# Performance work log

Hardware: AMD Instinct MI355X
Metric: run time of the kernel (lower is better)

The kernel has to match this reference:

```python
import jax, jax.numpy as jnp
import numpy as np

PILLAR_WH = np.array([0.16, 0.16], np.float32)
MAX_POINTS = 100
MAX_PILLARS = 12000
MIN_XYZ = np.array([-51.2, -51.2, -5.0], np.float32)
MAX_XYZ = np.array([51.2, 51.2, 3.0], np.float32)
PAD_VALUE = 0.0
NGRID = np.ceil((MAX_XYZ[:2] - MIN_XYZ[:2]) / PILLAR_WH).astype(np.int32)  # [640, 640]
WH_N = (2.0 * PILLAR_WH / (MAX_XYZ[:2] - MIN_XYZ[:2])).astype(np.float32)  # pillar size in normalized coords
MIN_XY_N = (MIN_XYZ[:2] / MAX_XYZ[:2]).astype(np.float32)  # = [-1, -1]


def setup_inputs() -> dict:
    key = jax.random.key(0)
    B, P = 4, 50000
    k1, k2, k3 = jax.random.split(key, 3)
    # x,y restricted to [-8, 8] m so occupied pillars (<=100x100=10000) <= max_pillars,
    # making the torch module's random pillar subsampling a deterministic no-op.
    xy = jax.random.uniform(k1, (B, P, 2), minval=-8.0, maxval=8.0, dtype=jnp.float32)
    z = jax.random.uniform(k2, (B, P, 1), minval=-5.0, maxval=3.0, dtype=jnp.float32)
    r = jax.random.uniform(k3, (B, P, 1), dtype=jnp.float32)
    return {"point_clouds": jnp.concatenate([xy, z, r], axis=-1)}


def _per_sample(pc, pidx):
    # pc: (P, 4) normalized points; pidx: (P,) int32 pillar ids
    P = pc.shape[0]
    u, inv = jnp.unique(pidx, size=MAX_PILLARS, fill_value=-1, return_inverse=True)
    counts = jax.ops.segment_sum(jnp.ones((P,), jnp.int32), inv, num_segments=MAX_PILLARS)
    sums = jax.ops.segment_sum(pc[:, :3], inv, num_segments=MAX_PILLARS)
    mean = sums / jnp.maximum(counts, 1).astype(pc.dtype)[:, None]
    # stable sort points by pillar id; rank = position within pillar
    order = jnp.argsort(inv)
    seg = inv[order]
    pts = pc[order]
    start = jnp.cumsum(counts) - counts  # exclusive prefix of counts
    rank = jnp.arange(P, dtype=jnp.int32) - start[seg]
    in_cap = rank < MAX_POINTS
    flat = jnp.where(in_cap, seg * MAX_POINTS + rank, MAX_PILLARS * MAX_POINTS)  # OOB -> dropped
    buf = jnp.zeros((MAX_PILLARS * MAX_POINTS, 4), pc.dtype).at[flat].set(pts, mode='drop')
    occ = jnp.zeros((MAX_PILLARS * MAX_POINTS,), bool).at[flat].set(True, mode='drop')
    buf = buf.reshape(MAX_PILLARS, MAX_POINTS, 4)
    occ = occ.reshape(MAX_PILLARS, MAX_POINTS)
    ij = jnp.stack([u % NGRID[0], u // NGRID[0]], axis=-1).astype(pc.dtype)
    centers = jnp.asarray(MIN_XY_N) + ij * jnp.asarray(WH_N) + jnp.asarray(WH_N) * 0.5
    feat_c = jnp.abs(buf[..., :3] - mean[:, None, :])  # |xyz - pillar mean|
    feat_p = centers[:, None, :] - buf[..., :2]        # pillar center offset
    out = jnp.concatenate([buf, feat_c, feat_p], axis=-1)  # (max_pillars, max_points, 9)
    out = jnp.where(occ[..., None], out, jnp.asarray(PAD_VALUE, pc.dtype))
    return out, u


def reference(point_clouds):
    pc = point_clouds
    xyz_n = 2.0 * (pc[..., :3] - jnp.asarray(MIN_XYZ)) / jnp.asarray(MAX_XYZ - MIN_XYZ) - 1.0
    pc_n = jnp.concatenate([xyz_n, pc[..., 3:]], axis=-1)
    ij = jnp.minimum(
        jnp.floor((xyz_n[..., :2] - jnp.asarray(MIN_XY_N)) / jnp.asarray(WH_N)),
        jnp.asarray(NGRID, xyz_n.dtype) - 1.0,
    ).astype(jnp.int32)
    pidx = ij[..., 1] * int(NGRID[0]) + ij[..., 0]
    out, pillars = jax.vmap(_per_sample)(pc_n, pidx)
    return out, pillars
```

## Files before the change

### kernel.cpp

```cpp
#include <hip/hip_runtime.h>

#define NB 4
#define GRID_X 640
#define NCELL (GRID_X*GRID_X)
#define NWORD (NCELL/32)
#define MAXPIL 12000
#define MAXPTS 100
#define SCAN_BLK 256
#define NBLKA (NWORD/SCAN_BLK)

typedef unsigned short u16;
typedef unsigned int   u32;

__device__ __forceinline__ float bf16rt(float f) {
    u32 u = __builtin_bit_cast(u32, f);
    u32 r = ((u + 0x7FFFu + ((u >> 16) & 1u)) >> 16) << 16;
    return __builtin_bit_cast(float, r);
}

__device__ __forceinline__ float opaquef(float x) { asm volatile("" : "+v"(x)); return x; }

#define R102 0.009765625f
#define RWH  320.000030517578125f
__device__ __host__ constexpr float WH_N_C() { return (2.0f*0.16f)/(51.2f-(-51.2f)); }

__device__ __forceinline__ float norm_x(float v) {
    float p = 2.0f*(v + 51.2f) * R102;
    return opaquef(p) - 1.0f;
}
__device__ __forceinline__ float norm_z(float v) {
    float p = 2.0f*(v + 5.0f) * 0.125f;
    return opaquef(p) - 1.0f;
}

__device__ __forceinline__ int cell_of(float xn, float yn) {
    float fx = fminf(fmaxf(floorf((xn + 1.0f) * RWH), 0.0f), 639.0f);
    float fy = fminf(fmaxf(floorf((yn + 1.0f) * RWH), 0.0f), 639.0f);
    return (int)fy * GRID_X + (int)fx;
}

__global__ void k_init(int4* __restrict__ zero4, int nz4,
                       float* __restrict__ pillars_f, int* __restrict__ slotCell, int npil) {
    int i = blockIdx.x*blockDim.x + threadIdx.x;
    if (i < nz4) zero4[i] = make_int4(0,0,0,0);
    if (i < npil) { pillars_f[i] = -1.0f; slotCell[i] = -1; }
}

__global__ void k_mask(const float4* __restrict__ pc, int P, u32* __restrict__ occMask) {
    int i = blockIdx.x*blockDim.x + threadIdx.x;
    if (i >= NB*P) return;
    float4 pt = pc[i];
    int cell = cell_of(norm_x(pt.x), norm_x(pt.y));
    int b = i / P;
    atomicOr(&occMask[b*NWORD + (cell >> 5)], 1u << (cell & 31));
}

__global__ void k_scanA(const u32* __restrict__ occMask, int* __restrict__ scanBlk) {
    __shared__ int lds[SCAN_BLK];
    int blk = blockIdx.x % NBLKA;
    int b   = blockIdx.x / NBLKA;
    int w   = blk*SCAN_BLK + threadIdx.x;
    lds[threadIdx.x] = __popc(occMask[b*NWORD + w]);
    __syncthreads();
    for (int d = SCAN_BLK/2; d > 0; d >>= 1) {
        if (threadIdx.x < d) lds[threadIdx.x] += lds[threadIdx.x + d];
        __syncthreads();
    }
    if (threadIdx.x == 0) scanBlk[b*NBLKA + blk] = lds[0];
}

__global__ void k_scanB(int* __restrict__ scanBlk) {
    int b = blockIdx.x;
    if (threadIdx.x == 0) {
        int acc = 0;
        for (int i = 0; i < NBLKA; i++) {
            int v = scanBlk[b*NBLKA + i];
            scanBlk[b*NBLKA + i] = acc;
            acc += v;
        }
    }
}

__global__ void k_scanC(const u32* __restrict__ occMask, const int* __restrict__ scanBlk,
                        int* __restrict__ wordPrefix, float* __restrict__ pillars_f,
                        int* __restrict__ slotCell) {
    __shared__ int lds[SCAN_BLK];
    int blk = blockIdx.x % NBLKA;
    int b   = blockIdx.x / NBLKA;
    int tid = threadIdx.x;
    int w   = blk*SCAN_BLK + tid;
    u32 m = occMask[b*NWORD + w];
    int pop = __popc(m);
    lds[tid] = pop;
    __syncthreads();
    for (int d = 1; d < SCAN_BLK; d <<= 1) {
        int t = (tid >= d) ? lds[tid - d] : 0;
        __syncthreads();
        lds[tid] += t;
        __syncthreads();
    }
    int prefix = scanBlk[b*NBLKA + blk] + lds[tid] - pop;
    wordPrefix[b*NWORD + w] = prefix;
    int wbase = w << 5;
    int slot = prefix;
    while (m) {
        int bit = __ffs(m) - 1;
        m &= m - 1;
        if (slot < MAXPIL) {
            int cell = wbase + bit;
            slotCell[b*MAXPIL + slot] = cell;
            pillars_f[b*MAXPIL + slot] = bf16rt((float)cell);
        }
        slot++;
    }
}

__global__ void k_scatter(const float4* __restrict__ pc, int P,
                          const u32* __restrict__ occMask, const int* __restrict__ wordPrefix,
                          int* __restrict__ slotCnt, u16* __restrict__ idx16) {
    int i = blockIdx.x*blockDim.x + threadIdx.x;
    if (i >= NB*P) return;
    int b = i / P;
    int p = i - b*P;
    float4 pt = pc[i];
    int cell = cell_of(norm_x(pt.x), norm_x(pt.y));
    int w = cell >> 5, bit = cell & 31;
    u32 m = occMask[b*NWORD + w];
    int slot = wordPrefix[b*NWORD + w] + __popc(m & ((1u << bit) - 1u));
    if (slot >= MAXPIL) return;
    int g = b*MAXPIL + slot;
    int pos = atomicAdd(&slotCnt[g], 1);
    if (pos < MAXPTS) idx16[(size_t)g*MAXPTS + pos] = (u16)p;
}

__global__ __launch_bounds__(64) void k_write(const float4* __restrict__ pc, int P,
                        const int* __restrict__ slotCell, const int* __restrict__ slotCnt,
                        const u16* __restrict__ idx16, float* __restrict__ out) {
    __shared__ __align__(16) float tile[MAXPTS*9];
    __shared__ int sIdx[MAXPTS];
    __shared__ float sx[MAXPTS], sy[MAXPTS], sz[MAXPTS], sr[MAXPTS];
    int g = blockIdx.x;
    int b = g / MAXPIL;
    int lane = threadIdx.x;
    float4* out4 = (float4*)out + (size_t)g*225;
    int u = slotCell[g];
    if (u < 0) {
        float4 z = make_float4(0.f,0.f,0.f,0.f);
        for (int i = lane; i < 225; i += 64) out4[i] = z;
        return;
    }
    int ntot = slotCnt[g];
    int n = min(ntot, MAXPTS);

    float4* t4 = (float4*)tile;
    for (int i = lane; i < 225; i += 64) t4[i] = make_float4(0.f,0.f,0.f,0.f);

    float ax = 0.f, ay = 0.f, az = 0.f;
    for (int j = lane; j < n; j += 64) {
        int p = idx16[(size_t)g*MAXPTS + j];
        sIdx[j] = p;
        float4 pt = pc[b*P + p];
        float xn = norm_x(pt.x);
        float yn = norm_x(pt.y);
        float zn = norm_z(pt.z);
        sx[j] = xn; sy[j] = yn; sz[j] = zn; sr[j] = pt.w;
        ax += xn; ay += yn; az += zn;
    }
    for (int msk = 1; msk < 64; msk <<= 1) {
        ax += __shfl_xor(ax, msk);
        ay += __shfl_xor(ay, msk);
        az += __shfl_xor(az, msk);
    }
    float den = (float)max(ntot, 1);
    float mx = ax/den, my = ay/den, mz = az/den;
    const float wh = WH_N_C();
    float cx = -1.0f + (float)(u % GRID_X)*wh + wh*0.5f;
    float cy = -1.0f + (float)(u / GRID_X)*wh + wh*0.5f;
    __syncthreads();

    for (int j = lane; j < n; j += 64) {
        int p = sIdx[j];
        int rk = 0;
        for (int k = 0; k < n; k++) rk += (sIdx[k] < p) ? 1 : 0;
        float xn = sx[j], yn = sy[j], zn = sz[j];
        float* e = &tile[rk*9];
        e[0] = xn; e[1] = yn; e[2] = zn; e[3] = sr[j];
        e[4] = fabsf(xn - mx); e[5] = fabsf(yn - my); e[6] = fabsf(zn - mz);
        e[7] = cx - xn; e[8] = cy - yn;
    }
    __syncthreads();
    for (int i = lane; i < 225; i += 64) out4[i] = t4[i];
}

extern "C" void kernel_launch(void* const* d_in, const int* in_sizes, int n_in,
                              void* d_out, int out_size, void* d_ws, size_t ws_size,
                              hipStream_t stream) {
    const float4* pc = (const float4*)d_in[0];
    int P = in_sizes[0] / (NB*4);
    float* out = (float*)d_out;
    float* pillars_f = out + (size_t)NB*MAXPIL*MAXPTS*9;

    u32* occMask   = (u32*)d_ws;
    int* slotCnt   = (int*)(occMask + NB*NWORD);
    int* wordPrefix= slotCnt + NB*MAXPIL;
    int* scanBlk   = wordPrefix + NB*NWORD;
    int* slotCell  = scanBlk + 256;
    u16* idx16     = (u16*)(slotCell + NB*MAXPIL);

    int nzero = NB*NWORD + NB*MAXPIL;
    int nz4 = nzero / 4;
    int initThreads = nz4 > NB*MAXPIL ? nz4 : NB*MAXPIL;

    k_init<<<(initThreads+255)/256, 256, 0, stream>>>((int4*)occMask, nz4, pillars_f, slotCell, NB*MAXPIL);
    k_mask<<<(NB*P+255)/256, 256, 0, stream>>>(pc, P, occMask);
    k_scanA<<<NB*NBLKA, SCAN_BLK, 0, stream>>>(occMask, scanBlk);
    k_scanB<<<NB, 64, 0, stream>>>(scanBlk);
    k_scanC<<<NB*NBLKA, SCAN_BLK, 0, stream>>>(occMask, scanBlk, wordPrefix, pillars_f, slotCell);
    k_scatter<<<(NB*P+255)/256, 256, 0, stream>>>(pc, P, occMask, wordPrefix, slotCnt, idx16);
    k_write<<<NB*MAXPIL, 64, 0, stream>>>(pc, P, slotCell, slotCnt, idx16, out);
}
```

Measured before the change: 227.1 us.

## Merge scan into single-block kernel, zero output upfront, one thread per pillar

The three-kernel scan becomes one kernel per batch with 256 threads, each handling 50 words serially, which cuts two launches. The whole output is zeroed in one bulk pass at the start. The write kernel now uses one thread per pillar instead of a 64-lane block per pillar, computing ranks serially and writing 9-float rows straight to global memory with no LDS tile. The risks are long serial loops per thread (O(n^2) rank, scan over 50 words with only 4 blocks) and uncoalesced scattered row stores.

After: 293.9 us. 29.4% more time.

```diff
diff --git a/kernel.cpp b/kernel.cpp
--- a/kernel.cpp
+++ b/kernel.cpp
@@ -6,8 +6,7 @@
 #define NWORD (NCELL/32)
 #define MAXPIL 12000
 #define MAXPTS 100
-#define SCAN_BLK 256
-#define NBLKA (NWORD/SCAN_BLK)
+#define WPT (NWORD/256)
 
 typedef unsigned short u16;
 typedef unsigned int   u32;
@@ -39,11 +38,10 @@
     return (int)fy * GRID_X + (int)fx;
 }
 
-__global__ void k_init(int4* __restrict__ zero4, int nz4,
-                       float* __restrict__ pillars_f, int* __restrict__ slotCell, int npil) {
+__global__ void k_zero(float4* __restrict__ out4, int n4, int4* __restrict__ ws4, int nw4) {
     int i = blockIdx.x*blockDim.x + threadIdx.x;
-    if (i < nz4) zero4[i] = make_int4(0,0,0,0);
-    if (i < npil) { pillars_f[i] = -1.0f; slotCell[i] = -1; }
+    if (i < n4) out4[i] = make_float4(0.f,0.f,0.f,0.f);
+    if (i < nw4) ws4[i] = make_int4(0,0,0,0);
 }
 
 __global__ void k_mask(const float4* __restrict__ pc, int P, u32* __restrict__ occMask) {
@@ -55,63 +53,44 @@
     atomicOr(&occMask[b*NWORD + (cell >> 5)], 1u << (cell & 31));
 }
 
-__global__ void k_scanA(const u32* __restrict__ occMask, int* __restrict__ scanBlk) {
-    __shared__ int lds[SCAN_BLK];
-    int blk = blockIdx.x % NBLKA;
-    int b   = blockIdx.x / NBLKA;
-    int w   = blk*SCAN_BLK + threadIdx.x;
-    lds[threadIdx.x] = __popc(occMask[b*NWORD + w]);
+__global__ __launch_bounds__(256) void k_scan(const u32* __restrict__ occMask,
+                                              int* __restrict__ wordPrefix,
+                                              float* __restrict__ pillars_f,
+                                              int* __restrict__ slotCell) {
+    __shared__ int part[256];
+    int b = blockIdx.x, t = threadIdx.x;
+    for (int s = t; s < MAXPIL; s += 256) {
+        pillars_f[b*MAXPIL + s] = -1.0f;
+        slotCell[b*MAXPIL + s] = -1;
+    }
+    int base = b*NWORD + t*WPT;
+    int sum = 0;
+    #pragma unroll 10
+    for (int i = 0; i < WPT; i++) sum += __popc(occMask[base + i]);
+    part[t] = sum;
     __syncthreads();
-    for (int d = SCAN_BLK/2; d > 0; d >>= 1) {
-        if (threadIdx.x < d) lds[threadIdx.x] += lds[threadIdx.x + d];
+    for (int d = 1; d < 256; d <<= 1) {
+        int v = (t >= d) ? part[t - d] : 0;
+        __syncthreads();
+        part[t] += v;
         __syncthreads();
     }
-    if (threadIdx.x == 0) scanBlk[b*NBLKA + blk] = lds[0];
-}
-
-__global__ void k_scanB(int* __restrict__ scanBlk) {
-    int b = blockIdx.x;
-    if (threadIdx.x == 0) {
-        int acc = 0;
-        for (int i = 0; i < NBLKA; i++) {
-            int v = scanBlk[b*NBLKA + i];
-            scanBlk[b*NBLKA + i] = acc;
-            acc += v;
+    int prefix = part[t] - sum;
+    __syncthreads();
+    for (int i = 0; i < WPT; i++) {
+        u32 m = occMask[base + i];
+        wordPrefix[b*NWORD + t*WPT + i] = prefix;
+        int wbase = (t*WPT + i) << 5;
+        while (m) {
+            int bit = __ffs(m) - 1;
+            m &= m - 1;
+            if (prefix < MAXPIL) {
+                int cell = wbase + bit;
+                slotCell[b*MAXPIL + prefix] = cell;
+                pillars_f[b*MAXPIL + prefix] = bf16rt((float)cell);
+            }
+            prefix++;
         }
-    }
-}
-
-__global__ void k_scanC(const u32* __restrict__ occMask, const int* __restrict__ scanBlk,
-                        int* __restrict__ wordPrefix, float* __restrict__ pillars_f,
-                        int* __restrict__ slotCell) {
-    __shared__ int lds[SCAN_BLK];
-    int blk = blockIdx.x % NBLKA;
-    int b   = blockIdx.x / NBLKA;
-    int tid = threadIdx.x;
-    int w   = blk*SCAN_BLK + tid;
-    u32 m = occMask[b*NWORD + w];
-    int pop = __popc(m);
-    lds[tid] = pop;
-    __syncthreads();
-    for (int d = 1; d < SCAN_BLK; d <<= 1) {
-        int t = (tid >= d) ? lds[tid - d] : 0;
-        __syncthreads();
-        lds[tid] += t;
-        __syncthreads();
-    }
-    int prefix = scanBlk[b*NBLKA + blk] + lds[tid] - pop;
-    wordPrefix[b*NWORD + w] = prefix;
-    int wbase = w << 5;
-    int slot = prefix;
-    while (m) {
-        int bit = __ffs(m) - 1;
-        m &= m - 1;
-        if (slot < MAXPIL) {
-            int cell = wbase + bit;
-            slotCell[b*MAXPIL + slot] = cell;
-            pillars_f[b*MAXPIL + slot] = bf16rt((float)cell);
-        }
-        slot++;
     }
 }
 
@@ -133,63 +112,41 @@
     if (pos < MAXPTS) idx16[(size_t)g*MAXPTS + pos] = (u16)p;
 }
 
-__global__ __launch_bounds__(64) void k_write(const float4* __restrict__ pc, int P,
-                        const int* __restrict__ slotCell, const int* __restrict__ slotCnt,
-                        const u16* __restrict__ idx16, float* __restrict__ out) {
-    __shared__ __align__(16) float tile[MAXPTS*9];
-    __shared__ int sIdx[MAXPTS];
-    __shared__ float sx[MAXPTS], sy[MAXPTS], sz[MAXPTS], sr[MAXPTS];
-    int g = blockIdx.x;
+__global__ void k_rows(const float4* __restrict__ pc, int P,
+                       const int* __restrict__ slotCell, const int* __restrict__ slotCnt,
+                       const u16* __restrict__ idx16, float* __restrict__ out) {
+    int g = blockIdx.x*blockDim.x + threadIdx.x;
+    if (g >= NB*MAXPIL) return;
+    int u = slotCell[g];
+    if (u < 0) return;
     int b = g / MAXPIL;
-    int lane = threadIdx.x;
-    float4* out4 = (float4*)out + (size_t)g*225;
-    int u = slotCell[g];
-    if (u < 0) {
-        float4 z = make_float4(0.f,0.f,0.f,0.f);
-        for (int i = lane; i < 225; i += 64) out4[i] = z;
-        return;
-    }
     int ntot = slotCnt[g];
     int n = min(ntot, MAXPTS);
-
-    float4* t4 = (float4*)tile;
-    for (int i = lane; i < 225; i += 64) t4[i] = make_float4(0.f,0.f,0.f,0.f);
+    const u16* lst = idx16 + (size_t)g*MAXPTS;
 
     float ax = 0.f, ay = 0.f, az = 0.f;
-    for (int j = lane; j < n; j += 64) {
-        int p = idx16[(size_t)g*MAXPTS + j];
-        sIdx[j] = p;
-        float4 pt = pc[b*P + p];
-        float xn = norm_x(pt.x);
-        float yn = norm_x(pt.y);
-        float zn = norm_z(pt.z);
-        sx[j] = xn; sy[j] = yn; sz[j] = zn; sr[j] = pt.w;
-        ax += xn; ay += yn; az += zn;
-    }
-    for (int msk = 1; msk < 64; msk <<= 1) {
-        ax += __shfl_xor(ax, msk);
-        ay += __shfl_xor(ay, msk);
-        az += __shfl_xor(az, msk);
+    for (int j = 0; j < n; j++) {
+        float4 pt = pc[b*P + lst[j]];
+        ax += norm_x(pt.x); ay += norm_x(pt.y); az += norm_z(pt.z);
     }
     float den = (float)max(ntot, 1);
     float mx = ax/den, my = ay/den, mz = az/den;
     const float wh = WH_N_C();
     float cx = -1.0f + (float)(u % GRID_X)*wh + wh*0.5f;
     float cy = -1.0f + (float)(u / GRID_X)*wh + wh*0.5f;
-    __syncthreads();
 
-    for (int j = lane; j < n; j += 64) {
-        int p = sIdx[j];
+    float* pil = out + (size_t)g*900;
+    for (int j = 0; j < n; j++) {
+        int p = lst[j];
         int rk = 0;
-        for (int k = 0; k < n; k++) rk += (sIdx[k] < p) ? 1 : 0;
-        float xn = sx[j], yn = sy[j], zn = sz[j];
-        float* e = &tile[rk*9];
-        e[0] = xn; e[1] = yn; e[2] = zn; e[3] = sr[j];
+        for (int k = 0; k < n; k++) rk += (lst[k] < (u16)p) ? 1 : 0;
+        float4 pt = pc[b*P + p];
+        float xn = norm_x(pt.x), yn = norm_x(pt.y), zn = norm_z(pt.z);
+        float* e = pil + rk*9;
+        e[0] = xn; e[1] = yn; e[2] = zn; e[3] = pt.w;
         e[4] = fabsf(xn - mx); e[5] = fabsf(yn - my); e[6] = fabsf(zn - mz);
         e[7] = cx - xn; e[8] = cy - yn;
     }
-    __syncthreads();
-    for (int i = lane; i < 225; i += 64) out4[i] = t4[i];
 }
 
 extern "C" void kernel_launch(void* const* d_in, const int* in_sizes, int n_in,
@@ -203,19 +160,15 @@
     u32* occMask   = (u32*)d_ws;
     int* slotCnt   = (int*)(occMask + NB*NWORD);
     int* wordPrefix= slotCnt + NB*MAXPIL;
-    int* scanBlk   = wordPrefix + NB*NWORD;
-    int* slotCell  = scanBlk + 256;
+    int* slotCell  = wordPrefix + NB*NWORD;
     u16* idx16     = (u16*)(slotCell + NB*MAXPIL);
 
-    int nzero = NB*NWORD + NB*MAXPIL;
-    int nz4 = nzero / 4;
-    int initThreads = nz4 > NB*MAXPIL ? nz4 : NB*MAXPIL;
+    const int nOut4 = NB*MAXPIL*MAXPTS*9/4;
+    const int nWs4  = (NB*NWORD + NB*MAXPIL)/4;
 
-    k_init<<<(initThreads+255)/256, 256, 0, stream>>>((int4*)occMask, nz4, pillars_f, slotCell, NB*MAXPIL);
+    k_zero<<<(nOut4+255)/256, 256, 0, stream>>>((float4*)out, nOut4, (int4*)occMask, nWs4);
     k_mask<<<(NB*P+255)/256, 256, 0, stream>>>(pc, P, occMask);
-    k_scanA<<<NB*NBLKA, SCAN_BLK, 0, stream>>>(occMask, scanBlk);
-    k_scanB<<<NB, 64, 0, stream>>>(scanBlk);
-    k_scanC<<<NB*NBLKA, SCAN_BLK, 0, stream>>>(occMask, scanBlk, wordPrefix, pillars_f, slotCell);
+    k_scan<<<NB, 256, 0, stream>>>(occMask, wordPrefix, pillars_f, slotCell);
     k_scatter<<<(NB*P+255)/256, 256, 0, stream>>>(pc, P, occMask, wordPrefix, slotCnt, idx16);
-    k_write<<<NB*MAXPIL, 64, 0, stream>>>(pc, P, slotCell, slotCnt, idx16, out);
+    k_rows<<<(NB*MAXPIL+255)/256, 256, 0, stream>>>(pc, P, slotCell, slotCnt, idx16, out);
 }
```

## Fold block-offset scan into scanC, cache pillar ids, trim write-kernel LDS zeroing

Applied to the files above, without the earlier changes.

Drops the single-threaded k_scanB launch by having each k_scanC block sum the preceding block totals with a wavefront shuffle reduction. k_mask now stores each point's cell index, so k_scatter reads it instead of recomputing from the point cloud. k_write no longer stages normalized coordinates in LDS or zeroes the whole tile. It re-reads points from global memory, zero-fills only the unused tail, and pads with zeros on the store. This removes a serial launch and some LDS traffic, at the cost of an extra point-id buffer and repeated global gathers of points.

Measured after the change: 243.5 us. +7.2%, slower.

```diff
diff --git a/kernel.cpp b/kernel.cpp
--- a/kernel.cpp
+++ b/kernel.cpp
@@ -6,8 +6,7 @@
 #define NWORD (NCELL/32)
 #define MAXPIL 12000
 #define MAXPTS 100
-#define SCAN_BLK 256
-#define NBLKA (NWORD/SCAN_BLK)
+#define NBLKA (NWORD/256)
 
 typedef unsigned short u16;
 typedef unsigned int   u32;
@@ -39,91 +38,86 @@
     return (int)fy * GRID_X + (int)fx;
 }
 
-__global__ void k_init(int4* __restrict__ zero4, int nz4,
+__global__ void k_init(int4* __restrict__ ws4, int nw4,
                        float* __restrict__ pillars_f, int* __restrict__ slotCell, int npil) {
     int i = blockIdx.x*blockDim.x + threadIdx.x;
-    if (i < nz4) zero4[i] = make_int4(0,0,0,0);
+    if (i < nw4) ws4[i] = make_int4(0,0,0,0);
     if (i < npil) { pillars_f[i] = -1.0f; slotCell[i] = -1; }
 }
 
-__global__ void k_mask(const float4* __restrict__ pc, int P, u32* __restrict__ occMask) {
+__global__ void k_mask(const float4* __restrict__ pc, int P,
+                       u32* __restrict__ occMask, u32* __restrict__ pidxBuf) {
     int i = blockIdx.x*blockDim.x + threadIdx.x;
     if (i >= NB*P) return;
     float4 pt = pc[i];
     int cell = cell_of(norm_x(pt.x), norm_x(pt.y));
     int b = i / P;
     atomicOr(&occMask[b*NWORD + (cell >> 5)], 1u << (cell & 31));
-}
-
-__global__ void k_scanA(const u32* __restrict__ occMask, int* __restrict__ scanBlk) {
-    __shared__ int lds[SCAN_BLK];
+    pidxBuf[i] = (u32)cell;
+}
+
+__global__ void k_scanA(const u32* __restrict__ occMask, int* __restrict__ blockSums) {
+    __shared__ int lds[256];
     int blk = blockIdx.x % NBLKA;
     int b   = blockIdx.x / NBLKA;
-    int w   = blk*SCAN_BLK + threadIdx.x;
+    int w   = blk*256 + threadIdx.x;
     lds[threadIdx.x] = __popc(occMask[b*NWORD + w]);
     __syncthreads();
-    for (int d = SCAN_BLK/2; d > 0; d >>= 1) {
+    for (int d = 128; d > 0; d >>= 1) {
         if (threadIdx.x < d) lds[threadIdx.x] += lds[threadIdx.x + d];
         __syncthreads();
     }
-    if (threadIdx.x == 0) scanBlk[b*NBLKA + blk] = lds[0];
-}
-
-__global__ void k_scanB(int* __restrict__ scanBlk) {
-    int b = blockIdx.x;
-    if (threadIdx.x == 0) {
-        int acc = 0;
-        for (int i = 0; i < NBLKA; i++) {
-            int v = scanBlk[b*NBLKA + i];
-            scanBlk[b*NBLKA + i] = acc;
-            acc += v;
-        }
-    }
-}
-
-__global__ void k_scanC(const u32* __restrict__ occMask, const int* __restrict__ scanBlk,
+    if (threadIdx.x == 0) blockSums[b*NBLKA + blk] = lds[0];
+}
+
+__global__ __launch_bounds__(256) void k_scanC(const u32* __restrict__ occMask,
+                        const int* __restrict__ blockSums,
                         int* __restrict__ wordPrefix, float* __restrict__ pillars_f,
                         int* __restrict__ slotCell) {
-    __shared__ int lds[SCAN_BLK];
+    __shared__ int lds[256];
+    __shared__ int offs;
     int blk = blockIdx.x % NBLKA;
     int b   = blockIdx.x / NBLKA;
     int tid = threadIdx.x;
-    int w   = blk*SCAN_BLK + tid;
+    int w   = blk*256 + tid;
     u32 m = occMask[b*NWORD + w];
     int pop = __popc(m);
     lds[tid] = pop;
-    __syncthreads();
-    for (int d = 1; d < SCAN_BLK; d <<= 1) {
+    if (tid < 64) {
+        int v = (tid < blk) ? blockSums[b*NBLKA + tid] : 0;
+        for (int msk = 1; msk < 64; msk <<= 1) v += __shfl_xor(v, msk);
+        if (tid == 0) offs = v;
+    }
+    __syncthreads();
+    for (int d = 1; d < 256; d <<= 1) {
         int t = (tid >= d) ? lds[tid - d] : 0;
         __syncthreads();
         lds[tid] += t;
         __syncthreads();
     }
-    int prefix = scanBlk[b*NBLKA + blk] + lds[tid] - pop;
+    int prefix = offs + lds[tid] - pop;
     wordPrefix[b*NWORD + w] = prefix;
     int wbase = w << 5;
-    int slot = prefix;
     while (m) {
         int bit = __ffs(m) - 1;
         m &= m - 1;
-        if (slot < MAXPIL) {
+        if (prefix < MAXPIL) {
             int cell = wbase + bit;
-            slotCell[b*MAXPIL + slot] = cell;
-            pillars_f[b*MAXPIL + slot] = bf16rt((float)cell);
+            slotCell[b*MAXPIL + prefix] = cell;
+            pillars_f[b*MAXPIL + prefix] = bf16rt((float)cell);
         }
-        slot++;
-    }
-}
-
-__global__ void k_scatter(const float4* __restrict__ pc, int P,
+        prefix++;
+    }
+}
+
+__global__ void k_scatter(int P, const u32* __restrict__ pidxBuf,
                           const u32* __restrict__ occMask, const int* __restrict__ wordPrefix,
                           int* __restrict__ slotCnt, u16* __restrict__ idx16) {
     int i = blockIdx.x*blockDim.x + threadIdx.x;
     if (i >= NB*P) return;
     int b = i / P;
     int p = i - b*P;
-    float4 pt = pc[i];
-    int cell = cell_of(norm_x(pt.x), norm_x(pt.y));
+    int cell = (int)pidxBuf[i];
     int w = cell >> 5, bit = cell & 31;
     u32 m = occMask[b*NWORD + w];
     int slot = wordPrefix[b*NWORD + w] + __popc(m & ((1u << bit) - 1u));
@@ -136,11 +130,9 @@
 __global__ __launch_bounds__(64) void k_write(const float4* __restrict__ pc, int P,
                         const int* __restrict__ slotCell, const int* __restrict__ slotCnt,
                         const u16* __restrict__ idx16, float* __restrict__ out) {
-    __shared__ __align__(16) float tile[MAXPTS*9];
+    __shared__ __align__(16) float tile[MAXPTS*9 + 4];
     __shared__ int sIdx[MAXPTS];
-    __shared__ float sx[MAXPTS], sy[MAXPTS], sz[MAXPTS], sr[MAXPTS];
     int g = blockIdx.x;
-    int b = g / MAXPIL;
     int lane = threadIdx.x;
     float4* out4 = (float4*)out + (size_t)g*225;
     int u = slotCell[g];
@@ -149,22 +141,18 @@
         for (int i = lane; i < 225; i += 64) out4[i] = z;
         return;
     }
+    int b = g / MAXPIL;
     int ntot = slotCnt[g];
     int n = min(ntot, MAXPTS);
-
-    float4* t4 = (float4*)tile;
-    for (int i = lane; i < 225; i += 64) t4[i] = make_float4(0.f,0.f,0.f,0.f);
+    const u16* lst = idx16 + (size_t)g*MAXPTS;
+
+    for (int j = lane; j < n; j += 64) sIdx[j] = lst[j];
+    __syncthreads();
 
     float ax = 0.f, ay = 0.f, az = 0.f;
     for (int j = lane; j < n; j += 64) {
-        int p = idx16[(size_t)g*MAXPTS + j];
-        sIdx[j] = p;
-        float4 pt = pc[b*P + p];
-        float xn = norm_x(pt.x);
-        float yn = norm_x(pt.y);
-        float zn = norm_z(pt.z);
-        sx[j] = xn; sy[j] = yn; sz[j] = zn; sr[j] = pt.w;
-        ax += xn; ay += yn; az += zn;
+        float4 pt = pc[b*P + sIdx[j]];
+        ax += norm_x(pt.x); ay += norm_x(pt.y); az += norm_z(pt.z);
     }
     for (int msk = 1; msk < 64; msk <<= 1) {
         ax += __shfl_xor(ax, msk);
@@ -176,20 +164,26 @@
     const float wh = WH_N_C();
     float cx = -1.0f + (float)(u % GRID_X)*wh + wh*0.5f;
     float cy = -1.0f + (float)(u / GRID_X)*wh + wh*0.5f;
-    __syncthreads();
 
     for (int j = lane; j < n; j += 64) {
         int p = sIdx[j];
         int rk = 0;
         for (int k = 0; k < n; k++) rk += (sIdx[k] < p) ? 1 : 0;
-        float xn = sx[j], yn = sy[j], zn = sz[j];
-        float* e = &tile[rk*9];
-        e[0] = xn; e[1] = yn; e[2] = zn; e[3] = sr[j];
+        float4 pt = pc[b*P + p];
+        float xn = norm_x(pt.x), yn = norm_x(pt.y), zn = norm_z(pt.z);
+        float* e = tile + rk*9;
+        e[0] = xn; e[1] = yn; e[2] = zn; e[3] = pt.w;
         e[4] = fabsf(xn - mx); e[5] = fabsf(yn - my); e[6] = fabsf(zn - mz);
         e[7] = cx - xn; e[8] = cy - yn;
     }
-    __syncthreads();
-    for (int i = lane; i < 225; i += 64) out4[i] = t4[i];
+    int nd = n*9;
+    int nf4 = (nd + 3) >> 2;
+    if (lane < nf4*4 - nd) tile[nd + lane] = 0.f;
+    __syncthreads();
+
+    float4* t4 = (float4*)tile;
+    float4 z = make_float4(0.f,0.f,0.f,0.f);
+    for (int i = lane; i < 225; i += 64) out4[i] = (i < nf4) ? t4[i] : z;
 }
 
 extern "C" void kernel_launch(void* const* d_in, const int* in_sizes, int n_in,
@@ -203,19 +197,19 @@
     u32* occMask   = (u32*)d_ws;
     int* slotCnt   = (int*)(occMask + NB*NWORD);
     int* wordPrefix= slotCnt + NB*MAXPIL;
-    int* scanBlk   = wordPrefix + NB*NWORD;
-    int* slotCell  = scanBlk + 256;
-    u16* idx16     = (u16*)(slotCell + NB*MAXPIL);
-
-    int nzero = NB*NWORD + NB*MAXPIL;
-    int nz4 = nzero / 4;
-    int initThreads = nz4 > NB*MAXPIL ? nz4 : NB*MAXPIL;
-
-    k_init<<<(initThreads+255)/256, 256, 0, stream>>>((int4*)occMask, nz4, pillars_f, slotCell, NB*MAXPIL);
-    k_mask<<<(NB*P+255)/256, 256, 0, stream>>>(pc, P, occMask);
-    k_scanA<<<NB*NBLKA, SCAN_BLK, 0, stream>>>(occMask, scanBlk);
-    k_scanB<<<NB, 64, 0, stream>>>(scanBlk);
-    k_scanC<<<NB*NBLKA, SCAN_BLK, 0, stream>>>(occMask, scanBlk, wordPrefix, pillars_f, slotCell);
-    k_scatter<<<(NB*P+255)/256, 256, 0, stream>>>(pc, P, occMask, wordPrefix, slotCnt, idx16);
+    int* slotCell  = wordPrefix + NB*NWORD;
+    int* blockSums = slotCell + NB*MAXPIL;
+    u32* pidxBuf   = (u32*)(blockSums + 256);
+    u16* idx16     = (u16*)(pidxBuf + NB*P);
+
+    const int nWs4 = (NB*NWORD + NB*MAXPIL)/4;
+    const int npil = NB*MAXPIL;
+    int initThreads = npil > nWs4 ? npil : nWs4;
+
+    k_init<<<(initThreads+255)/256, 256, 0, stream>>>((int4*)occMask, nWs4, pillars_f, slotCell, npil);
+    k_mask<<<(NB*P+255)/256, 256, 0, stream>>>(pc, P, occMask, pidxBuf);
+    k_scanA<<<NB*NBLKA, 256, 0, stream>>>(occMask, blockSums);
+    k_scanC<<<NB*NBLKA, 256, 0, stream>>>(occMask, blockSums, wordPrefix, pillars_f, slotCell);
+    k_scatter<<<(NB*P+255)/256, 256, 0, stream>>>(P, pidxBuf, occMask, wordPrefix, slotCnt, idx16);
     k_write<<<NB*MAXPIL, 64, 0, stream>>>(pc, P, slotCell, slotCnt, idx16, out);
 }
```
